# Kernel optimization log

Measured on AMD Instinct MI355X. Metric: run time of the kernel, lower is better.

The kernel has to match this reference:

```python
import jax, jax.numpy as jnp
import numpy as np

S, B, D, H, L = 512, 512, 300, 256, 3

def setup_inputs() -> dict:
    key = jax.random.key(0)
    ks = jax.random.split(key, 9)
    sc = 0.02
    return {
        "x": jax.random.normal(ks[0], (S, B, D), dtype=jnp.float32),
        "fW_ih0": jax.random.normal(ks[1], (D, H), dtype=jnp.float32) * sc,
        "fW_ih": jax.random.normal(ks[2], (L - 1, H, H), dtype=jnp.float32) * sc,
        "fW_hh": jax.random.normal(ks[3], (L, H, H), dtype=jnp.float32) * sc,
        "fb": jnp.zeros((L, H), dtype=jnp.float32),
        "bW_ih0": jax.random.normal(ks[4], (D, H), dtype=jnp.float32) * sc,
        "bW_ih": jax.random.normal(ks[5], (L - 1, H, H), dtype=jnp.float32) * sc,
        "bW_hh": jax.random.normal(ks[6], (L, H, H), dtype=jnp.float32) * sc,
        "bb": jnp.zeros((L, H), dtype=jnp.float32),
    }

def _run_rnn(x, W_ih0, W_ih, W_hh, b):
    # x: [S, B, D]; stacked vanilla tanh RNN with L layers.
    batch = x.shape[1]
    h0 = jnp.zeros((L, batch, H), dtype=x.dtype)

    def step(h, x_t):  # h: [L, B, H], x_t: [B, D]
        inp = x_t
        new_h = []
        for l in range(L):
            Wih = W_ih0 if l == 0 else W_ih[l - 1]
            hl = jnp.tanh(inp @ Wih + h[l] @ W_hh[l] + b[l])
            new_h.append(hl)
            inp = hl
        return jnp.stack(new_h, axis=0), None

    h_final, _ = jax.lax.scan(step, h0, x)
    return h_final  # [L, B, H]

def reference(x, fW_ih0, fW_ih, fW_hh, fb, bW_ih0, bW_ih, bW_hh, bb):
    hf = _run_rnn(x, fW_ih0, fW_ih, fW_hh, fb)          # forward direction
    hb = _run_rnn(x[::-1], bW_ih0, bW_ih, bW_hh, bb)    # backward direction
    return jnp.concatenate((hf[-1], hb[-1]), axis=-1)   # [B, 2H]
```

## Files before the change

### kernel.cpp

```cpp
#include <hip/hip_runtime.h>
#include <cstdint>
#include <cstddef>


#define SEQ   512
#define BATCH 512
#define DIN   300
#define HDIM  256
#define NT    512
#define CH    64
#define NCH   (SEQ / CH)
#define NSLOT (NCH + 2)
#define TS    16
#define ZTILE 131072

typedef _Float16 f16x8 __attribute__((ext_vector_type(8)));
typedef __fp16   fp16x2 __attribute__((ext_vector_type(2)));
typedef float    f32x4 __attribute__((ext_vector_type(4)));

#define WIH0_E 0
#define WHH_E  163840
#define WIHN_E 557056
#define HC_BYTE   1638400
#define HB_BYTE   3211264
#define Z0_BYTE   (HB_BYTE + 67108864)
#define Z1_BYTE   (Z0_BYTE + 268435456)
#define Z2_BYTE   (Z1_BYTE + 67108864)
#define RING_E    8388608ull

static __device__ __forceinline__ uint16_t f16bits(_Float16 h) {
    union { _Float16 h; uint16_t u; } v; v.h = h; return v.u;
}
static __device__ __forceinline__ uint32_t pk2(float a, float b) {
    union { fp16x2 h; uint32_t u; } v; v.h = __builtin_amdgcn_cvt_pkrtz(a, b); return v.u;
}
static __device__ __forceinline__ int swz(int row, int col) {
    return (row * 256 + col) ^ ((row & 7) << 3);
}

static __device__ __forceinline__ void aload8(f16x8 r[8], const _Float16* p, size_t stepE) {
    const _Float16* p0 = p;
    const _Float16* p1 = p + stepE;
    const _Float16* p2 = p + 2 * stepE;
    const _Float16* p3 = p + 3 * stepE;
    const _Float16* p4 = p + 4 * stepE;
    const _Float16* p5 = p + 5 * stepE;
    const _Float16* p6 = p + 6 * stepE;
    const _Float16* p7 = p + 7 * stepE;
    asm volatile(
        "global_load_dwordx4 %0, %8, off\n\t"
        "global_load_dwordx4 %1, %9, off\n\t"
        "global_load_dwordx4 %2, %10, off\n\t"
        "global_load_dwordx4 %3, %11, off\n\t"
        "global_load_dwordx4 %4, %12, off\n\t"
        "global_load_dwordx4 %5, %13, off\n\t"
        "global_load_dwordx4 %6, %14, off\n\t"
        "global_load_dwordx4 %7, %15, off"
        : "=&v"(r[0]), "=&v"(r[1]), "=&v"(r[2]), "=&v"(r[3]),
          "=&v"(r[4]), "=&v"(r[5]), "=&v"(r[6]), "=&v"(r[7])
        : "v"(p0), "v"(p1), "v"(p2), "v"(p3), "v"(p4), "v"(p5), "v"(p6), "v"(p7)
        : "memory");
}
static __device__ __forceinline__ void adrain() {
    asm volatile("s_waitcnt vmcnt(0)" ::: "memory");
    __builtin_amdgcn_sched_barrier(0);
}

__global__ void rnn_prep(const float* __restrict__ fW_ih0, const float* __restrict__ fW_ih,
                         const float* __restrict__ fW_hh,  const float* __restrict__ bW_ih0,
                         const float* __restrict__ bW_ih,  const float* __restrict__ bW_hh,
                         _Float16* __restrict__ wf)
{
    const int gid = blockIdx.x * 256 + threadIdx.x;
    const int d = gid / 51200;
    const int r = gid - d * 51200;
    const int lane = r & 63;
    const float* Wih0 = d ? bW_ih0 : fW_ih0;
    const float* Wih  = d ? bW_ih  : fW_ih;
    const float* Whh  = d ? bW_hh  : fW_hh;
    _Float16 vals[8];
    size_t dstE;
    if (r < 10240) {
        const int ck = r >> 6, ct = ck / 10, kt = ck - ct * 10;
        const int col = ct * 16 + (lane & 15);
        const int k0  = kt * 32 + (lane >> 4) * 8;
        #pragma unroll
        for (int e = 0; e < 8; ++e) {
            const int k = k0 + e;
            vals[e] = (k < 300) ? (_Float16)Wih0[(size_t)k * 256 + col] : (_Float16)0.f;
        }
        dstE = (size_t)WIH0_E + (size_t)d * 81920 + (size_t)r * 8;
    } else if (r < 34816) {
        const int rr = r - 10240, l = rr / 8192, r2 = rr - l * 8192;
        const int ck = r2 >> 6, ct = ck >> 3, kt = ck & 7;
        const int col = ct * 16 + (lane & 15);
        const int k0  = kt * 32 + (lane >> 4) * 8;
        #pragma unroll
        for (int e = 0; e < 8; ++e)
            vals[e] = (_Float16)Whh[((size_t)(l * 256 + k0 + e)) * 256 + col];
        dstE = (size_t)WHH_E + (size_t)(d * 3 + l) * 65536 + (size_t)r2 * 8;
    } else {
        const int rr = r - 34816, ln = rr / 8192, r2 = rr - ln * 8192;
        const int ck = r2 >> 6, ct = ck >> 3, kt = ck & 7;
        const int col = ct * 16 + (lane & 15);
        const int k0  = kt * 32 + (lane >> 4) * 8;
        #pragma unroll
        for (int e = 0; e < 8; ++e)
            vals[e] = (_Float16)Wih[((size_t)(ln * 256 + k0 + e)) * 256 + col];
        dstE = (size_t)WIHN_E + (size_t)(d * 2 + ln) * 65536 + (size_t)r2 * 8;
    }
    *(f16x8*)(wf + dstE) = *(const f16x8*)vals;
}

__global__ __attribute__((amdgpu_flat_work_group_size(NT, NT)))
void rnn_gemm0(const float* __restrict__ x, const _Float16* __restrict__ wih0,
               const float* __restrict__ fb, const float* __restrict__ bb,
               uint16_t* __restrict__ z0)
{
    __shared__ uint16_t Xl[2][16 * 332];
    const int tid = threadIdx.x, lane = tid & 63, w = tid >> 6;
    const int colw = lane & 15, rq = lane >> 4, rq8 = rq * 8;
    const int ct0 = w * 2;
    const int sg = blockIdx.x >> 5, rb = blockIdx.x & 31;
    const int b0 = rb * 16;
    const size_t chunk = ((size_t)(rb * 8 + w) * 64 + lane) * 8;

    int rs[5], cc2[5]; bool pv[5];
    #pragma unroll
    for (int b = 0; b < 5; ++b) {
        const int p = tid + b * NT;
        pv[b] = p < 2400;
        const int r = p / 150;
        rs[b] = r; cc2[b] = (p - r * 150) * 2;
    }

    float bv[2][2];
    #pragma unroll
    for (int dd = 0; dd < 2; ++dd)
        #pragma unroll
        for (int c = 0; c < 2; ++c)
            bv[dd][c] = (dd ? bb : fb)[(ct0 + c) * 16 + colw];

    for (int p = tid; p < 320; p += NT) {
        const int bu = p / 160, q = p - bu * 160;
        const int r = q / 10, cc = 300 + (q - r * 10) * 2;
        *(uint32_t*)&Xl[bu][r * 332 + cc] = 0;
    }
    {
        const float* xs = x + ((size_t)(sg * TS) * BATCH + b0) * DIN;
        #pragma unroll
        for (int b = 0; b < 5; ++b) if (pv[b]) {
            const float2 v = *(const float2*)(xs + (size_t)rs[b] * DIN + cc2[b]);
            *(uint32_t*)&Xl[0][rs[b] * 332 + cc2[b]] = pk2(v.x, v.y);
        }
    }
    __syncthreads();

    #pragma unroll 1
    for (int si = 0; si < TS; ++si) {
        const int s = sg * TS + si;
        const int buf = si & 1;
        const bool last = (si == TS - 1);

        {
            f32x4 a0 = (f32x4){bv[0][0], bv[0][0], bv[0][0], bv[0][0]};
            f32x4 a1 = (f32x4){bv[0][1], bv[0][1], bv[0][1], bv[0][1]};
            #pragma unroll
            for (int kt = 0; kt < 10; ++kt) {
                const f16x8 wv0 = *(const f16x8*)(wih0 + (((size_t)ct0 * 10 + kt) * 64 + lane) * 8);
                const f16x8 wv1 = *(const f16x8*)(wih0 + (((size_t)(ct0 + 1) * 10 + kt) * 64 + lane) * 8);
                const f16x8 a = *(const f16x8*)&Xl[buf][colw * 332 + kt * 32 + rq8];
                a0 = __builtin_amdgcn_mfma_f32_16x16x32_f16(a, wv0, a0, 0, 0, 0);
                a1 = __builtin_amdgcn_mfma_f32_16x16x32_f16(a, wv1, a1, 0, 0, 0);
            }
            uint4 sv;
            sv.x = pk2(a0[0], a0[1]); sv.y = pk2(a0[2], a0[3]);
            sv.z = pk2(a1[0], a1[1]); sv.w = pk2(a1[2], a1[3]);
            *(uint4*)(z0 + (size_t)s * ZTILE + chunk) = sv;
        }

        float2 xr[5];
        if (!last) {
            const float* xs = x + ((size_t)(s + 1) * BATCH + b0) * DIN;
            #pragma unroll
            for (int b = 0; b < 5; ++b) if (pv[b])
                xr[b] = *(const float2*)(xs + (size_t)rs[b] * DIN + cc2[b]);
        }

        {
            f32x4 a0 = (f32x4){bv[1][0], bv[1][0], bv[1][0], bv[1][0]};
            f32x4 a1 = (f32x4){bv[1][1], bv[1][1], bv[1][1], bv[1][1]};
            #pragma unroll
            for (int kt = 0; kt < 10; ++kt) {
                const f16x8 wv0 = *(const f16x8*)(wih0 + 81920 + (((size_t)ct0 * 10 + kt) * 64 + lane) * 8);
                const f16x8 wv1 = *(const f16x8*)(wih0 + 81920 + (((size_t)(ct0 + 1) * 10 + kt) * 64 + lane) * 8);
                const f16x8 a = *(const f16x8*)&Xl[buf][colw * 332 + kt * 32 + rq8];
                a0 = __builtin_amdgcn_mfma_f32_16x16x32_f16(a, wv0, a0, 0, 0, 0);
                a1 = __builtin_amdgcn_mfma_f32_16x16x32_f16(a, wv1, a1, 0, 0, 0);
            }
            uint4 sv;
            sv.x = pk2(a0[0], a0[1]); sv.y = pk2(a0[2], a0[3]);
            sv.z = pk2(a1[0], a1[1]); sv.w = pk2(a1[2], a1[3]);
            *(uint4*)(z0 + ((size_t)SEQ + (SEQ - 1 - s)) * ZTILE + chunk) = sv;
        }

        if (!last) {
            #pragma unroll
            for (int b = 0; b < 5; ++b) if (pv[b])
                *(uint32_t*)&Xl[buf ^ 1][rs[b] * 332 + cc2[b]] = pk2(xr[b].x, xr[b].y);
        }

        __builtin_amdgcn_sched_barrier(0);
        asm volatile("s_waitcnt lgkmcnt(0)" ::: "memory");
        __builtin_amdgcn_s_barrier();
        __builtin_amdgcn_sched_barrier(0);
    }
}

template<int L>
__device__ __forceinline__ void rec_run(const _Float16* whh_all, const _Float16* wihn_all,
                                        const uint16_t* zsrc, uint16_t* zdst,
                                        uint16_t* hcarry, const float* fb, const float* bb,
                                        float* out, int d, int i, int cs, uint16_t* Hb)
{
    const int tid = threadIdx.x, lane = tid & 63, w = tid >> 6;
    const int colw = lane & 15, rq = lane >> 4, rq8 = rq * 8;
    const int ct0 = w * 2;
    const int grow0 = i * 16;

    const _Float16* whh = whh_all + (size_t)(d * 3 + L) * 65536;
    f16x8 wh0[8], wh1[8];
    aload8(wh0, whh + ((size_t)ct0 * 8 * 64 + lane) * 8, 512);
    aload8(wh1, whh + ((size_t)(ct0 + 1) * 8 * 64 + lane) * 8, 512);
    f16x8 wn0[8], wn1[8];
    float bn0 = 0.f, bn1 = 0.f;
    if constexpr (L < 2) {
        const _Float16* wnx = wihn_all + (size_t)(d * 2 + L) * 65536;
        aload8(wn0, wnx + ((size_t)ct0 * 8 * 64 + lane) * 8, 512);
        aload8(wn1, wnx + ((size_t)(ct0 + 1) * 8 * 64 + lane) * 8, 512);
        const float* bnx = (d ? bb : fb) + (L + 1) * HDIM;
        bn0 = bnx[ct0 * 16 + colw];
        bn1 = bnx[(ct0 + 1) * 16 + colw];
    }
    adrain();

    for (int p = tid; p < 4096; p += NT) ((uint32_t*)Hb)[p] = 0;
    __syncthreads();
    if (cs > 0) {
        const uint16_t* hc = hcarry + (size_t)(d * 3 + L) * 131072;
        const int row = tid >> 5, c8 = (tid & 31) * 8;
        *(uint4*)&Hb[4096 + ((row * 256 + c8) ^ ((row & 7) << 3))] =
            *(const uint4*)(hc + (size_t)(grow0 + row) * 256 + c8);
    }
    __syncthreads();

    const size_t zoff = ((size_t)(i * 8 + w) * 64 + lane) * 8;

    uint4 zp[4];
    #pragma unroll
    for (int j = 0; j < 4; ++j)
        zp[j] = *(const uint4*)(zsrc + (size_t)j * ZTILE + zoff);

    f32x4 anp0 = {}, anp1 = {};

    #pragma unroll 1
    for (int k0 = 0; k0 < CH; k0 += 4) {
        #pragma unroll
        for (int u = 0; u < 4; ++u) {
            const int k = k0 + u;
            const int cur = u & 1, prv = cur ^ 1;

            f32x4 ar0, ar1;
            {
                union { uint4 v; _Float16 h[8]; } zz; zz.v = zp[u];
                ar0 = (f32x4){(float)zz.h[0], (float)zz.h[1], (float)zz.h[2], (float)zz.h[3]};
                ar1 = (f32x4){(float)zz.h[4], (float)zz.h[5], (float)zz.h[6], (float)zz.h[7]};
            }
            {
                const int kp = (k + 4 < CH) ? (k + 4) : (CH - 1);
                zp[u] = *(const uint4*)(zsrc + (size_t)kp * ZTILE + zoff);
            }

            f16x8 ah[8];
            #pragma unroll
            for (int kt = 0; kt < 8; ++kt)
                ah[kt] = *(const f16x8*)&Hb[(prv << 12) + swz(colw, kt * 32 + rq8)];

            f32x4 an0, an1;
            if constexpr (L < 2) {
                an0 = (f32x4){bn0, bn0, bn0, bn0};
                an1 = (f32x4){bn1, bn1, bn1, bn1};
                #pragma unroll
                for (int kt = 0; kt < 8; ++kt) {
                    ar0 = __builtin_amdgcn_mfma_f32_16x16x32_f16(ah[kt], wh0[kt], ar0, 0, 0, 0);
                    ar1 = __builtin_amdgcn_mfma_f32_16x16x32_f16(ah[kt], wh1[kt], ar1, 0, 0, 0);
                    an0 = __builtin_amdgcn_mfma_f32_16x16x32_f16(ah[kt], wn0[kt], an0, 0, 0, 0);
                    an1 = __builtin_amdgcn_mfma_f32_16x16x32_f16(ah[kt], wn1[kt], an1, 0, 0, 0);
                }
            } else {
                f32x4 arB0 = {}, arB1 = {};
                #pragma unroll
                for (int kt = 0; kt < 4; ++kt) {
                    ar0  = __builtin_amdgcn_mfma_f32_16x16x32_f16(ah[kt],     wh0[kt],     ar0,  0, 0, 0);
                    ar1  = __builtin_amdgcn_mfma_f32_16x16x32_f16(ah[kt],     wh1[kt],     ar1,  0, 0, 0);
                    arB0 = __builtin_amdgcn_mfma_f32_16x16x32_f16(ah[4 + kt], wh0[4 + kt], arB0, 0, 0, 0);
                    arB1 = __builtin_amdgcn_mfma_f32_16x16x32_f16(ah[4 + kt], wh1[4 + kt], arB1, 0, 0, 0);
                }
                ar0 = ar0 + arB0;
                ar1 = ar1 + arB1;
            }

            if constexpr (L < 2) {
                if (k >= 2) {
                    uint4 sv;
                    sv.x = pk2(anp0[0], anp0[1]); sv.y = pk2(anp0[2], anp0[3]);
                    sv.z = pk2(anp1[0], anp1[1]); sv.w = pk2(anp1[2], anp1[3]);
                    *(uint4*)(zdst + (size_t)(k - 2) * ZTILE + zoff) = sv;
                }
            }

            float hv[8];
            #pragma unroll
            for (int q = 0; q < 8; ++q) {
                const float S = (q < 4) ? ar0[q] : ar1[q - 4];
                const float e = __builtin_amdgcn_exp2f(S * 2.885390081777927f);
                const float r = __builtin_amdgcn_rcpf(e + 1.f);
                hv[q] = __builtin_fmaf(-2.f, r, 1.f);
            }
            #pragma unroll
            for (int q = 0; q < 8; ++q) {
                const int c = q >> 2, j = q & 3;
                Hb[(cur << 12) + swz(rq * 4 + j, (ct0 + c) * 16 + colw)] = f16bits((_Float16)hv[q]);
            }
            if (L == 2 && cs == NCH - 1 && k == CH - 1) {
                #pragma unroll
                for (int q = 0; q < 8; ++q) {
                    const int c = q >> 2, j = q & 3;
                    out[(size_t)(grow0 + rq * 4 + j) * 512 + d * 256 + (ct0 + c) * 16 + colw] = hv[q];
                }
            }

            if constexpr (L < 2) { anp0 = an0; anp1 = an1; }

            __builtin_amdgcn_sched_barrier(0);
            asm volatile("s_waitcnt lgkmcnt(0)" ::: "memory");
            __builtin_amdgcn_s_barrier();
            __builtin_amdgcn_sched_barrier(0);
        }
    }

    if constexpr (L < 2) {
        {
            uint4 sv;
            sv.x = pk2(anp0[0], anp0[1]); sv.y = pk2(anp0[2], anp0[3]);
            sv.z = pk2(anp1[0], anp1[1]); sv.w = pk2(anp1[2], anp1[3]);
            *(uint4*)(zdst + (size_t)(CH - 2) * ZTILE + zoff) = sv;
        }
        f32x4 an0 = (f32x4){bn0, bn0, bn0, bn0};
        f32x4 an1 = (f32x4){bn1, bn1, bn1, bn1};
        #pragma unroll
        for (int kt = 0; kt < 8; ++kt) {
            const f16x8 ah = *(const f16x8*)&Hb[(1 << 12) + swz(colw, kt * 32 + rq8)];
            an0 = __builtin_amdgcn_mfma_f32_16x16x32_f16(ah, wn0[kt], an0, 0, 0, 0);
            an1 = __builtin_amdgcn_mfma_f32_16x16x32_f16(ah, wn1[kt], an1, 0, 0, 0);
        }
        uint4 sv;
        sv.x = pk2(an0[0], an0[1]); sv.y = pk2(an0[2], an0[3]);
        sv.z = pk2(an1[0], an1[1]); sv.w = pk2(an1[2], an1[3]);
        *(uint4*)(zdst + (size_t)(CH - 1) * ZTILE + zoff) = sv;
    }
    {
        uint16_t* hc = hcarry + (size_t)(d * 3 + L) * 131072;
        const int row = tid >> 5, c8 = (tid & 31) * 8;
        *(uint4*)(hc + (size_t)(grow0 + row) * 256 + c8) =
            *(const uint4*)&Hb[4096 + ((row * 256 + c8) ^ ((row & 7) << 3))];
    }
}

__global__ __attribute__((amdgpu_flat_work_group_size(NT, NT), amdgpu_waves_per_eu(2)))
void rnn_rec(const _Float16* whh_all, const _Float16* wihn_all,
             uint16_t* z0, uint16_t* z1, uint16_t* z2,
             uint16_t* hcarry, const float* fb, const float* bb,
             float* out, int slot)
{
    __shared__ uint16_t Hb[2 * 4096];
    const int l = blockIdx.x >> 6, sub = blockIdx.x & 63;
    const int d = sub >> 5, i = sub & 31;
    const int cs = slot - l;
    if (cs < 0 || cs >= NCH) return;
    const size_t ringE = (size_t)((cs & 1) * 2 + d) * RING_E;
    if (l == 0) {
        const uint16_t* zs = z0 + ((size_t)d * SEQ + (size_t)cs * CH) * ZTILE;
        rec_run<0>(whh_all, wihn_all, zs, z1 + ringE, hcarry, fb, bb, out, d, i, cs, Hb);
    } else if (l == 1) {
        rec_run<1>(whh_all, wihn_all, z1 + ringE, z2 + ringE, hcarry, fb, bb, out, d, i, cs, Hb);
    } else {
        rec_run<2>(whh_all, wihn_all, z2 + ringE, nullptr, hcarry, fb, bb, out, d, i, cs, Hb);
    }
}

extern "C" void kernel_launch(void* const* d_in, const int* in_sizes, int n_in,
                              void* d_out, int out_size, void* d_ws, size_t ws_size,
                              hipStream_t stream)
{
    (void)in_sizes; (void)n_in; (void)out_size; (void)ws_size;
    const float* x      = (const float*)d_in[0];
    const float* fW_ih0 = (const float*)d_in[1];
    const float* fW_ih  = (const float*)d_in[2];
    const float* fW_hh  = (const float*)d_in[3];
    const float* fb     = (const float*)d_in[4];
    const float* bW_ih0 = (const float*)d_in[5];
    const float* bW_ih  = (const float*)d_in[6];
    const float* bW_hh  = (const float*)d_in[7];
    const float* bb     = (const float*)d_in[8];
    uint8_t* ws = (uint8_t*)d_ws;

    _Float16* wf     = (_Float16*)ws;
    uint16_t* hcarry = (uint16_t*)(ws + HC_BYTE);
    uint16_t* z0     = (uint16_t*)(ws + Z0_BYTE);
    uint16_t* z1     = (uint16_t*)(ws + Z1_BYTE);
    uint16_t* z2     = (uint16_t*)(ws + Z2_BYTE);
    const _Float16* whh  = wf + WHH_E;
    const _Float16* wihn = wf + WIHN_E;
    float* out = (float*)d_out;

    rnn_prep<<<400, 256, 0, stream>>>(fW_ih0, fW_ih, fW_hh, bW_ih0, bW_ih, bW_hh, wf);
    rnn_gemm0<<<1024, NT, 0, stream>>>(x, wf, fb, bb, z0);
    for (int s = 0; s < NSLOT; ++s)
        rnn_rec<<<192, NT, 0, stream>>>(whh, wihn, z0, z1, z2, hcarry, fb, bb, out, s);
}
```

Measured before the change: 734.9 us.

## Split next-layer input projection out of recurrence into separate pipelined blocks

The recurrent blocks for layers 0 and 1 previously also computed the next layer's input projection (h @ W_ih + b) inside the serial time loop, which doubled their MFMA work on the critical path. Now they only write h to a staging buffer. 64 extra blocks per launch run the input projection as a separate pipeline stage on the previous chunk, over 32 rows at a time. This shortens the per-step serial latency but lengthens the pipeline by two slots and adds an extra round trip of hidden states through global memory.

New measurement: 1.209 ms. 1.65x slower.

```diff
diff --git a/kernel.cpp b/kernel.cpp
--- a/kernel.cpp
+++ b/kernel.cpp
@@ -10,7 +10,7 @@
 #define NT    512
 #define CH    64
 #define NCH   (SEQ / CH)
-#define NSLOT (NCH + 2)
+#define NSLOT (NCH + 4)
 #define TS    16
 #define ZTILE 131072
 
@@ -18,15 +18,13 @@
 typedef __fp16   fp16x2 __attribute__((ext_vector_type(2)));
 typedef float    f32x4 __attribute__((ext_vector_type(4)));
 
-#define WIH0_E 0
 #define WHH_E  163840
 #define WIHN_E 557056
-#define HC_BYTE   1638400
-#define HB_BYTE   3211264
-#define Z0_BYTE   (HB_BYTE + 67108864)
-#define Z1_BYTE   (Z0_BYTE + 268435456)
-#define Z2_BYTE   (Z1_BYTE + 67108864)
-#define RING_E    8388608ull
+#define HC_BYTE 1638400
+#define Z0_BYTE 4194304
+#define Z1_BYTE (Z0_BYTE + 268435456)
+#define Z2_BYTE (Z1_BYTE + 67108864)
+#define HH_BYTE (Z2_BYTE + 67108864)
 
 static __device__ __forceinline__ uint16_t f16bits(_Float16 h) {
     union { _Float16 h; uint16_t u; } v; v.h = h; return v.u;
@@ -89,7 +87,7 @@
             const int k = k0 + e;
             vals[e] = (k < 300) ? (_Float16)Wih0[(size_t)k * 256 + col] : (_Float16)0.f;
         }
-        dstE = (size_t)WIH0_E + (size_t)d * 81920 + (size_t)r * 8;
+        dstE = (size_t)d * 81920 + (size_t)r * 8;
     } else if (r < 34816) {
         const int rr = r - 10240, l = rr / 8192, r2 = rr - l * 8192;
         const int ck = r2 >> 6, ct = ck >> 3, kt = ck & 7;
@@ -218,10 +216,10 @@
 }
 
 template<int L>
-__device__ __forceinline__ void rec_run(const _Float16* whh_all, const _Float16* wihn_all,
-                                        const uint16_t* zsrc, uint16_t* zdst,
-                                        uint16_t* hcarry, const float* fb, const float* bb,
-                                        float* out, int d, int i, int cs, uint16_t* Hb)
+__device__ __forceinline__ void rec_run(const _Float16* whh_all,
+                                        const uint16_t* zsrc, uint16_t* hhdst,
+                                        uint16_t* hcarry, float* out,
+                                        int d, int i, int cs, uint16_t* Hb)
 {
     const int tid = threadIdx.x, lane = tid & 63, w = tid >> 6;
     const int colw = lane & 15, rq = lane >> 4, rq8 = rq * 8;
@@ -232,16 +230,6 @@
     f16x8 wh0[8], wh1[8];
     aload8(wh0, whh + ((size_t)ct0 * 8 * 64 + lane) * 8, 512);
     aload8(wh1, whh + ((size_t)(ct0 + 1) * 8 * 64 + lane) * 8, 512);
-    f16x8 wn0[8], wn1[8];
-    float bn0 = 0.f, bn1 = 0.f;
-    if constexpr (L < 2) {
-        const _Float16* wnx = wihn_all + (size_t)(d * 2 + L) * 65536;
-        aload8(wn0, wnx + ((size_t)ct0 * 8 * 64 + lane) * 8, 512);
-        aload8(wn1, wnx + ((size_t)(ct0 + 1) * 8 * 64 + lane) * 8, 512);
-        const float* bnx = (d ? bb : fb) + (L + 1) * HDIM;
-        bn0 = bnx[ct0 * 16 + colw];
-        bn1 = bnx[(ct0 + 1) * 16 + colw];
-    }
     adrain();
 
     for (int p = tid; p < 4096; p += NT) ((uint32_t*)Hb)[p] = 0;
@@ -261,8 +249,6 @@
     for (int j = 0; j < 4; ++j)
         zp[j] = *(const uint4*)(zsrc + (size_t)j * ZTILE + zoff);
 
-    f32x4 anp0 = {}, anp1 = {};
-
     #pragma unroll 1
     for (int k0 = 0; k0 < CH; k0 += 4) {
         #pragma unroll
@@ -286,38 +272,16 @@
             for (int kt = 0; kt < 8; ++kt)
                 ah[kt] = *(const f16x8*)&Hb[(prv << 12) + swz(colw, kt * 32 + rq8)];
 
-            f32x4 an0, an1;
-            if constexpr (L < 2) {
-                an0 = (f32x4){bn0, bn0, bn0, bn0};
-                an1 = (f32x4){bn1, bn1, bn1, bn1};
-                #pragma unroll
-                for (int kt = 0; kt < 8; ++kt) {
-                    ar0 = __builtin_amdgcn_mfma_f32_16x16x32_f16(ah[kt], wh0[kt], ar0, 0, 0, 0);
-                    ar1 = __builtin_amdgcn_mfma_f32_16x16x32_f16(ah[kt], wh1[kt], ar1, 0, 0, 0);
-                    an0 = __builtin_amdgcn_mfma_f32_16x16x32_f16(ah[kt], wn0[kt], an0, 0, 0, 0);
-                    an1 = __builtin_amdgcn_mfma_f32_16x16x32_f16(ah[kt], wn1[kt], an1, 0, 0, 0);
-                }
-            } else {
-                f32x4 arB0 = {}, arB1 = {};
-                #pragma unroll
-                for (int kt = 0; kt < 4; ++kt) {
-                    ar0  = __builtin_amdgcn_mfma_f32_16x16x32_f16(ah[kt],     wh0[kt],     ar0,  0, 0, 0);
-                    ar1  = __builtin_amdgcn_mfma_f32_16x16x32_f16(ah[kt],     wh1[kt],     ar1,  0, 0, 0);
-                    arB0 = __builtin_amdgcn_mfma_f32_16x16x32_f16(ah[4 + kt], wh0[4 + kt], arB0, 0, 0, 0);
-                    arB1 = __builtin_amdgcn_mfma_f32_16x16x32_f16(ah[4 + kt], wh1[4 + kt], arB1, 0, 0, 0);
-                }
-                ar0 = ar0 + arB0;
-                ar1 = ar1 + arB1;
-            }
-
-            if constexpr (L < 2) {
-                if (k >= 2) {
-                    uint4 sv;
-                    sv.x = pk2(anp0[0], anp0[1]); sv.y = pk2(anp0[2], anp0[3]);
-                    sv.z = pk2(anp1[0], anp1[1]); sv.w = pk2(anp1[2], anp1[3]);
-                    *(uint4*)(zdst + (size_t)(k - 2) * ZTILE + zoff) = sv;
-                }
-            }
+            f32x4 arB0 = {}, arB1 = {};
+            #pragma unroll
+            for (int kt = 0; kt < 4; ++kt) {
+                ar0  = __builtin_amdgcn_mfma_f32_16x16x32_f16(ah[kt],     wh0[kt],     ar0,  0, 0, 0);
+                ar1  = __builtin_amdgcn_mfma_f32_16x16x32_f16(ah[kt],     wh1[kt],     ar1,  0, 0, 0);
+                arB0 = __builtin_amdgcn_mfma_f32_16x16x32_f16(ah[4 + kt], wh0[4 + kt], arB0, 0, 0, 0);
+                arB1 = __builtin_amdgcn_mfma_f32_16x16x32_f16(ah[4 + kt], wh1[4 + kt], arB1, 0, 0, 0);
+            }
+            ar0 = ar0 + arB0;
+            ar1 = ar1 + arB1;
 
             float hv[8];
             #pragma unroll
@@ -326,6 +290,12 @@
                 const float e = __builtin_amdgcn_exp2f(S * 2.885390081777927f);
                 const float r = __builtin_amdgcn_rcpf(e + 1.f);
                 hv[q] = __builtin_fmaf(-2.f, r, 1.f);
+            }
+            if constexpr (L < 2) {
+                uint4 sv;
+                sv.x = pk2(hv[0], hv[1]); sv.y = pk2(hv[2], hv[3]);
+                sv.z = pk2(hv[4], hv[5]); sv.w = pk2(hv[6], hv[7]);
+                *(uint4*)(hhdst + (size_t)k * ZTILE + zoff) = sv;
             }
             #pragma unroll
             for (int q = 0; q < 8; ++q) {
@@ -340,8 +310,6 @@
                 }
             }
 
-            if constexpr (L < 2) { anp0 = an0; anp1 = an1; }
-
             __builtin_amdgcn_sched_barrier(0);
             asm volatile("s_waitcnt lgkmcnt(0)" ::: "memory");
             __builtin_amdgcn_s_barrier();
@@ -349,26 +317,6 @@
         }
     }
 
-    if constexpr (L < 2) {
-        {
-            uint4 sv;
-            sv.x = pk2(anp0[0], anp0[1]); sv.y = pk2(anp0[2], anp0[3]);
-            sv.z = pk2(anp1[0], anp1[1]); sv.w = pk2(anp1[2], anp1[3]);
-            *(uint4*)(zdst + (size_t)(CH - 2) * ZTILE + zoff) = sv;
-        }
-        f32x4 an0 = (f32x4){bn0, bn0, bn0, bn0};
-        f32x4 an1 = (f32x4){bn1, bn1, bn1, bn1};
-        #pragma unroll
-        for (int kt = 0; kt < 8; ++kt) {
-            const f16x8 ah = *(const f16x8*)&Hb[(1 << 12) + swz(colw, kt * 32 + rq8)];
-            an0 = __builtin_amdgcn_mfma_f32_16x16x32_f16(ah, wn0[kt], an0, 0, 0, 0);
-            an1 = __builtin_amdgcn_mfma_f32_16x16x32_f16(ah, wn1[kt], an1, 0, 0, 0);
-        }
-        uint4 sv;
-        sv.x = pk2(an0[0], an0[1]); sv.y = pk2(an0[2], an0[3]);
-        sv.z = pk2(an1[0], an1[1]); sv.w = pk2(an1[2], an1[3]);
-        *(uint4*)(zdst + (size_t)(CH - 1) * ZTILE + zoff) = sv;
-    }
     {
         uint16_t* hc = hcarry + (size_t)(d * 3 + L) * 131072;
         const int row = tid >> 5, c8 = (tid & 31) * 8;
@@ -377,25 +325,133 @@
     }
 }
 
+__device__ __forceinline__ void an_run(const _Float16* wihn_all,
+                                       const uint16_t* hsrc, uint16_t* zdst,
+                                       const float* fb, const float* bb,
+                                       int lp, int d, int i16, uint16_t* Hl)
+{
+    const int tid = threadIdx.x, lane = tid & 63, w = tid >> 6;
+    const int colw = lane & 15, rq = lane >> 4, rq8 = rq * 8;
+    const int ct0 = w * 2;
+
+    const _Float16* wnx = wihn_all + (size_t)(d * 2 + lp) * 65536;
+    f16x8 wn0[8], wn1[8];
+    aload8(wn0, wnx + ((size_t)ct0 * 8 * 64 + lane) * 8, 512);
+    aload8(wn1, wnx + ((size_t)(ct0 + 1) * 8 * 64 + lane) * 8, 512);
+    adrain();
+    const float* bnx = (d ? bb : fb) + (lp + 1) * HDIM;
+    const float bn0 = bnx[ct0 * 16 + colw];
+    const float bn1 = bnx[(ct0 + 1) * 16 + colw];
+
+    size_t hoff[2], zo[2];
+    #pragma unroll
+    for (int m = 0; m < 2; ++m) {
+        hoff[m] = ((size_t)((i16 * 2 + m) * 8 + w) * 64 + lane) * 8;
+        zo[m]   = hoff[m];
+    }
+
+    #pragma unroll
+    for (int m = 0; m < 2; ++m) {
+        union { uint4 v; uint16_t s[8]; } hz;
+        hz.v = *(const uint4*)(hsrc + hoff[m]);
+        #pragma unroll
+        for (int q = 0; q < 8; ++q) {
+            const int c = q >> 2, j = q & 3;
+            Hl[swz(m * 16 + rq * 4 + j, (ct0 + c) * 16 + colw)] = hz.s[q];
+        }
+    }
+    __syncthreads();
+
+    #pragma unroll 1
+    for (int t = 0; t < CH; ++t) {
+        const int buf = t & 1;
+
+        uint4 hn[2];
+        if (t < CH - 1) {
+            #pragma unroll
+            for (int m = 0; m < 2; ++m)
+                hn[m] = *(const uint4*)(hsrc + (size_t)(t + 1) * ZTILE + hoff[m]);
+        }
+
+        f16x8 ah[2][8];
+        #pragma unroll
+        for (int m = 0; m < 2; ++m)
+            #pragma unroll
+            for (int kt = 0; kt < 8; ++kt)
+                ah[m][kt] = *(const f16x8*)&Hl[(buf << 13) + swz(m * 16 + colw, kt * 32 + rq8)];
+
+        f32x4 acc[2][2];
+        #pragma unroll
+        for (int m = 0; m < 2; ++m) {
+            acc[m][0] = (f32x4){bn0, bn0, bn0, bn0};
+            acc[m][1] = (f32x4){bn1, bn1, bn1, bn1};
+        }
+        #pragma unroll
+        for (int kt = 0; kt < 8; ++kt)
+            #pragma unroll
+            for (int m = 0; m < 2; ++m) {
+                acc[m][0] = __builtin_amdgcn_mfma_f32_16x16x32_f16(ah[m][kt], wn0[kt], acc[m][0], 0, 0, 0);
+                acc[m][1] = __builtin_amdgcn_mfma_f32_16x16x32_f16(ah[m][kt], wn1[kt], acc[m][1], 0, 0, 0);
+            }
+
+        if (t < CH - 1) {
+            #pragma unroll
+            for (int m = 0; m < 2; ++m) {
+                union { uint4 v; uint16_t s[8]; } hz; hz.v = hn[m];
+                #pragma unroll
+                for (int q = 0; q < 8; ++q) {
+                    const int c = q >> 2, j = q & 3;
+                    Hl[((buf ^ 1) << 13) + swz(m * 16 + rq * 4 + j, (ct0 + c) * 16 + colw)] = hz.s[q];
+                }
+            }
+        }
+
+        #pragma unroll
+        for (int m = 0; m < 2; ++m) {
+            uint4 sv;
+            sv.x = pk2(acc[m][0][0], acc[m][0][1]); sv.y = pk2(acc[m][0][2], acc[m][0][3]);
+            sv.z = pk2(acc[m][1][0], acc[m][1][1]); sv.w = pk2(acc[m][1][2], acc[m][1][3]);
+            *(uint4*)(zdst + (size_t)t * ZTILE + zo[m]) = sv;
+        }
+
+        __builtin_amdgcn_sched_barrier(0);
+        asm volatile("s_waitcnt lgkmcnt(0)" ::: "memory");
+        __builtin_amdgcn_s_barrier();
+        __builtin_amdgcn_sched_barrier(0);
+    }
+}
+
 __global__ __attribute__((amdgpu_flat_work_group_size(NT, NT), amdgpu_waves_per_eu(2)))
-void rnn_rec(const _Float16* whh_all, const _Float16* wihn_all,
-             uint16_t* z0, uint16_t* z1, uint16_t* z2,
-             uint16_t* hcarry, const float* fb, const float* bb,
-             float* out, int slot)
-{
-    __shared__ uint16_t Hb[2 * 4096];
-    const int l = blockIdx.x >> 6, sub = blockIdx.x & 63;
-    const int d = sub >> 5, i = sub & 31;
-    const int cs = slot - l;
-    if (cs < 0 || cs >= NCH) return;
-    const size_t ringE = (size_t)((cs & 1) * 2 + d) * RING_E;
-    if (l == 0) {
-        const uint16_t* zs = z0 + ((size_t)d * SEQ + (size_t)cs * CH) * ZTILE;
-        rec_run<0>(whh_all, wihn_all, zs, z1 + ringE, hcarry, fb, bb, out, d, i, cs, Hb);
-    } else if (l == 1) {
-        rec_run<1>(whh_all, wihn_all, z1 + ringE, z2 + ringE, hcarry, fb, bb, out, d, i, cs, Hb);
+void rnn_slot(const _Float16* whh_all, const _Float16* wihn_all,
+              uint16_t* z0, uint16_t* z1, uint16_t* z2,
+              uint16_t* hh, uint16_t* hcarry,
+              const float* fb, const float* bb, float* out, int slot)
+{
+    __shared__ uint16_t SH[2 * 8192];
+    if (blockIdx.x < 192) {
+        const int l = blockIdx.x >> 6, sub = blockIdx.x & 63;
+        const int d = sub >> 5, i = sub & 31;
+        const int cs = slot - 2 * l;
+        if (cs < 0 || cs >= NCH) return;
+        uint16_t* hhdst = hh + (size_t)(((l * 2 + d) * 2 + (cs & 1)) * 64) * ZTILE;
+        if (l == 0) {
+            const uint16_t* zs = z0 + ((size_t)d * SEQ + (size_t)cs * CH) * ZTILE;
+            rec_run<0>(whh_all, zs, hhdst, hcarry, out, d, i, cs, SH);
+        } else if (l == 1) {
+            const uint16_t* zs = z1 + (size_t)(((cs & 1) * 2 + d) * 64) * ZTILE;
+            rec_run<1>(whh_all, zs, hhdst, hcarry, out, d, i, cs, SH);
+        } else {
+            const uint16_t* zs = z2 + (size_t)(((cs & 1) * 2 + d) * 64) * ZTILE;
+            rec_run<2>(whh_all, zs, nullptr, hcarry, out, d, i, cs, SH);
+        }
     } else {
-        rec_run<2>(whh_all, wihn_all, z2 + ringE, nullptr, hcarry, fb, bb, out, d, i, cs, Hb);
+        const int a = blockIdx.x - 192;
+        const int lp = a >> 5, d = (a >> 4) & 1, i16 = a & 15;
+        const int ca = slot - 1 - 2 * lp;
+        if (ca < 0 || ca >= NCH) return;
+        const uint16_t* hsrc = hh + (size_t)(((lp * 2 + d) * 2 + (ca & 1)) * 64) * ZTILE;
+        uint16_t* zdst = (lp == 0 ? z1 : z2) + (size_t)(((ca & 1) * 2 + d) * 64) * ZTILE;
+        an_run(wihn_all, hsrc, zdst, fb, bb, lp, d, i16, SH);
     }
 }
 
@@ -420,6 +476,7 @@
     uint16_t* z0     = (uint16_t*)(ws + Z0_BYTE);
     uint16_t* z1     = (uint16_t*)(ws + Z1_BYTE);
     uint16_t* z2     = (uint16_t*)(ws + Z2_BYTE);
+    uint16_t* hh     = (uint16_t*)(ws + HH_BYTE);
     const _Float16* whh  = wf + WHH_E;
     const _Float16* wihn = wf + WIHN_E;
     float* out = (float*)d_out;
@@ -427,5 +484,5 @@
     rnn_prep<<<400, 256, 0, stream>>>(fW_ih0, fW_ih, fW_hh, bW_ih0, bW_ih, bW_hh, wf);
     rnn_gemm0<<<1024, NT, 0, stream>>>(x, wf, fb, bb, z0);
     for (int s = 0; s < NSLOT; ++s)
-        rnn_rec<<<192, NT, 0, stream>>>(whh, wihn, z0, z1, z2, hcarry, fb, bb, out, s);
-}
+        rnn_slot<<<256, NT, 0, stream>>>(whh, wihn, z0, z1, z2, hh, hcarry, fb, bb, out, s);
+}
```
